# Kernel tuning notes

Measured on AMD Instinct MI355X. Metric: run time of the kernel, lower is better.

## Reference

```python
import jax, jax.numpy as jnp
import numpy as np

B, SQ, SK, D, H = 8, 1024, 1024, 1024, 16
DH = D // H  # attention head size = 64
LN_EPS = 1e-5


def _layer_norm(x, g, b):
    m = jnp.mean(x, axis=-1, keepdims=True)
    v = jnp.mean(jnp.square(x - m), axis=-1, keepdims=True)
    return (x - m) * jax.lax.rsqrt(v + LN_EPS) * g + b


def setup_inputs() -> dict:
    key = jax.random.key(0)
    ks = jax.random.split(key, 12)
    s = 0.02
    return {
        "hidden_states": jax.random.normal(ks[0], (B, SQ, D), jnp.float32),
        "context": jax.random.normal(ks[1], (B, SK, D), jnp.float32),
        "Wq": jax.random.normal(ks[2], (D, D), jnp.float32) * s,
        "bq": jnp.zeros((D,), jnp.float32),
        "Wk": jax.random.normal(ks[3], (D, D), jnp.float32) * s,
        "bk": jnp.zeros((D,), jnp.float32),
        "Wv": jax.random.normal(ks[4], (D, D), jnp.float32) * s,
        "bv": jnp.zeros((D,), jnp.float32),
        "Wobs": jax.random.normal(ks[5], (D, D), jnp.float32) * s,
        "bobs": jnp.zeros((D,), jnp.float32),
        "Wmat": jax.random.normal(ks[6], (D, D), jnp.float32) * s,
        "bmat": jnp.zeros((D,), jnp.float32),
        "ln_g": jnp.ones((D,), jnp.float32),
        "ln_b": jnp.zeros((D,), jnp.float32),
    }


def reference(hidden_states, context, Wq, bq, Wk, bk, Wv, bv,
              Wobs, bobs, Wmat, bmat, ln_g, ln_b):
    # QKV projections (torch Linear: x @ W.T + b)
    q = hidden_states @ Wq.T + bq            # [B, SQ, D]
    k = context @ Wk.T + bk                  # [B, SK, D]
    v = context @ Wv.T + bv                  # [B, SK, D]

    # ---- Guide_Block: single-head SDPA over full D, then linear->ReLU->LN ----
    # (dropout is identity in eval mode)
    score = jnp.einsum('bqd,bkd->bqk', q, k) / np.sqrt(D)   # [B, SQ, SK]
    attn = jax.nn.softmax(score, axis=-1)
    gctx = jnp.einsum('bqk,bkd->bqd', attn, v)              # [B, SQ, D]
    new_q = _layer_norm(jax.nn.relu(gctx @ Wobs.T + bobs), ln_g, ln_b)
    new_k = _layer_norm(jax.nn.relu(k @ Wmat.T + bmat), ln_g, ln_b)

    # ---- Multi-head attention with guided q/k and original v ----
    qh = new_q.reshape(B, SQ, H, DH).transpose(0, 2, 1, 3)  # [B, H, SQ, DH]
    kh = new_k.reshape(B, SK, H, DH).transpose(0, 2, 1, 3)
    vh = v.reshape(B, SK, H, DH).transpose(0, 2, 1, 3)
    scores = jnp.einsum('bhqd,bhkd->bhqk', qh, kh) / np.sqrt(DH)
    probs = jax.nn.softmax(scores, axis=-1)                 # attn dropout = identity (eval)
    out = jnp.einsum('bhqk,bhkd->bhqd', probs, vh)          # [B, H, SQ, DH]
    return out.transpose(0, 2, 1, 3).reshape(B, SQ, D)
```

## Files before the change

kernel.cpp:

```cpp
#include <hip/hip_runtime.h>
#include <hip/hip_bf16.h>

#define DEV __device__ __forceinline__

using bf16x8 = __attribute__((ext_vector_type(8))) short;
using f32x4  = __attribute__((ext_vector_type(4))) float;
using f32x16 = __attribute__((ext_vector_type(16))) float;

#define MFMA16(a, b, c) __builtin_amdgcn_mfma_f32_16x16x32_bf16((a), (b), (c), 0, 0, 0)
#define MFMA32(a, b, c) __builtin_amdgcn_mfma_f32_32x32x16_bf16((a), (b), (c), 0, 0, 0)

#define GLOAD_LDS16(gp, lp)                                                        \
  __builtin_amdgcn_global_load_lds(                                               \
      (__attribute__((address_space(1))) unsigned int*)(gp),                      \
      (__attribute__((address_space(3))) unsigned int*)(lp), 16, 0, 0)

DEV float b2f(unsigned short u) {
  union { float f; unsigned u; } x; x.u = ((unsigned)u) << 16; return x.f;
}
DEV unsigned short f2b(float f) {
  union { float f; unsigned u; } x; x.f = f;
  unsigned r = x.u + 0x7FFFu + ((x.u >> 16) & 1u);
  return (unsigned short)(r >> 16);
}
DEV unsigned short f2b_trunc(float f) {
  union { float f; unsigned u; } x; x.f = f;
  return (unsigned short)(x.u >> 16);
}

__global__ __launch_bounds__(256) void detect_kernel(
    const unsigned short* __restrict__ hs, int* __restrict__ flag) {
  __shared__ int red[4];
  const int t = threadIdx.x;
  const ushort4* p = (const ushort4*)hs;
  int cnt = 0;
#pragma unroll
  for (int j = 0; j < 16; j++) {
    ushort4 u = p[j * 256 + t];
    cnt += (((u.x >> 7) & 0xFF) == 0xFF) + (((u.y >> 7) & 0xFF) == 0xFF) +
           (((u.z >> 7) & 0xFF) == 0xFF) + (((u.w >> 7) & 0xFF) == 0xFF);
  }
#pragma unroll
  for (int off = 32; off >= 1; off >>= 1) cnt += __shfl_xor(cnt, off, 64);
  if ((t & 63) == 0) red[t >> 6] = cnt;
  __syncthreads();
  if (t == 0) flag[0] = (red[0] + red[1] + red[2] + red[3] >= 4) ? 1 : 0;
}

__global__ __launch_bounds__(256) void convert2_kernel(
    const void* __restrict__ s0, const void* __restrict__ s1,
    unsigned short* __restrict__ d0, unsigned short* __restrict__ d1,
    const int* __restrict__ flag) {
  const int bid = blockIdx.x;
  const void* src;
  unsigned short* dst;
  long off;
  if (bid < 8192) { src = s0; dst = d0; off = (long)bid * 1024; }
  else            { src = s1; dst = d1; off = (long)(bid - 8192) * 1024; }
  const long i = off + threadIdx.x * 4;
  ushort4 o;
  if (*flag) {
    float4 f = ((const float4*)src)[i >> 2];
    o.x = f2b(f.x); o.y = f2b(f.y); o.z = f2b(f.z); o.w = f2b(f.w);
  } else {
    o = ((const ushort4*)src)[i >> 2];
  }
  ((ushort4*)dst)[i >> 2] = o;
}

__global__ __launch_bounds__(256) void convert_w_kernel(
    const void* __restrict__ s0, const void* __restrict__ s1,
    const void* __restrict__ s2, const void* __restrict__ s3,
    const void* __restrict__ s4, unsigned short* __restrict__ dst,
    const int* __restrict__ flag) {
  const void* srcs[5] = {s0, s1, s2, s3, s4};
  const void* src = srcs[blockIdx.y];
  unsigned short* d = dst + (long)blockIdx.y * 1048576;
  const int i = (blockIdx.x * 256 + threadIdx.x) * 4;
  ushort4 o;
  if (*flag) {
    float4 f = ((const float4*)src)[i >> 2];
    o.x = f2b(f.x); o.y = f2b(f.y); o.z = f2b(f.z); o.w = f2b(f.w);
  } else {
    o = ((const ushort4*)src)[i >> 2];
  }
  ((ushort4*)d)[i >> 2] = o;
}

__global__ __launch_bounds__(256) void convert_vec_kernel(
    const void* __restrict__ s0, const void* __restrict__ s1,
    const void* __restrict__ s2, const void* __restrict__ s3,
    const void* __restrict__ s4, const void* __restrict__ s5,
    const void* __restrict__ s6, unsigned short* __restrict__ dst,
    const int* __restrict__ flag) {
  const void* srcs[7] = {s0, s1, s2, s3, s4, s5, s6};
  const void* src = srcs[blockIdx.x];
  unsigned short* d = dst + blockIdx.x * 1024;
  const int i = threadIdx.x * 4;
  ushort4 o;
  if (*flag) {
    float4 f = ((const float4*)src)[i >> 2];
    o.x = f2b(f.x); o.y = f2b(f.y); o.z = f2b(f.z); o.w = f2b(f.w);
  } else {
    o = ((const ushort4*)src)[i >> 2];
  }
  ((ushort4*)d)[i >> 2] = o;
}

template <int RELU, int OUTBF16, int BIAS, int SPLIT>
__global__ __launch_bounds__(256, 2) void gemm_bt_kernel(
    const unsigned short* __restrict__ A, const unsigned short* __restrict__ B,
    const unsigned short* __restrict__ bias, void* __restrict__ Cv,
    void* __restrict__ Cv2, int M, int N, int K, long sA_, long sB_, long sC_,
    float scale) {
  __shared__ unsigned short sA[2][128 * 32];
  __shared__ unsigned short sB[2][128 * 32];
  const int t = threadIdx.x;
  const int wave = t >> 6, lane = t & 63;
  const int quad = lane >> 4, col = lane & 15;
  const int wm = wave >> 1, wn = wave & 1;
  const long zb = blockIdx.z;
  const unsigned short* Ab = A + zb * sA_ + (long)blockIdx.x * 128 * K;
  const unsigned short* Bb = B + zb * sB_ + (long)blockIdx.y * 128 * K;
  const int r0 = t >> 2;
  const int c0 = (t & 3) * 8;

  f32x4 zz = {0.f, 0.f, 0.f, 0.f};
  f32x4 acc[4][4];
#pragma unroll
  for (int i = 0; i < 4; i++)
#pragma unroll
    for (int j = 0; j < 4; j++) acc[i][j] = zz;

  for (int k0 = 0; k0 < K; k0 += 64) {
    __syncthreads();
#pragma unroll
    for (int p = 0; p < 2; p++) {
      GLOAD_LDS16(Ab + (long)r0 * K + k0 + p * 32 + c0,        &sA[p][t * 8]);
      GLOAD_LDS16(Ab + (long)(64 + r0) * K + k0 + p * 32 + c0, &sA[p][2048 + t * 8]);
      GLOAD_LDS16(Bb + (long)r0 * K + k0 + p * 32 + c0,        &sB[p][t * 8]);
      GLOAD_LDS16(Bb + (long)(64 + r0) * K + k0 + p * 32 + c0, &sB[p][2048 + t * 8]);
    }
    __syncthreads();
#pragma unroll
    for (int p = 0; p < 2; p++) {
      bf16x8 af[4], bfr[4];
#pragma unroll
      for (int mi = 0; mi < 4; mi++)
        af[mi] = *(const bf16x8*)&sA[p][(wm * 64 + mi * 16 + col) * 32 + quad * 8];
#pragma unroll
      for (int ni = 0; ni < 4; ni++)
        bfr[ni] = *(const bf16x8*)&sB[p][(wn * 64 + ni * 16 + col) * 32 + quad * 8];
#pragma unroll
      for (int mi = 0; mi < 4; mi++)
#pragma unroll
        for (int ni = 0; ni < 4; ni++)
          acc[mi][ni] = MFMA16(af[mi], bfr[ni], acc[mi][ni]);
    }
  }

  const int Rm = blockIdx.x * 128 + wm * 64;
  const int Cn = blockIdx.y * 128 + wn * 64;
  float bs[4];
#pragma unroll
  for (int ni = 0; ni < 4; ni++)
    bs[ni] = BIAS ? b2f(bias[Cn + ni * 16 + col]) : 0.f;

  unsigned short* Cb = (unsigned short*)Cv;
  int Nw = N, cadj = 0;
  if (SPLIT) {
    Nw = N >> 1;
    if (blockIdx.y >= (gridDim.y >> 1)) { Cb = (unsigned short*)Cv2; cadj = Nw; }
  }
#pragma unroll
  for (int mi = 0; mi < 4; mi++)
#pragma unroll
    for (int ni = 0; ni < 4; ni++)
#pragma unroll
      for (int r = 0; r < 4; r++) {
        int rr = Rm + mi * 16 + quad * 4 + r;
        int cc = Cn + ni * 16 + col;
        float v = acc[mi][ni][r] * scale + bs[ni];
        if (RELU) v = fmaxf(v, 0.f);
        if (OUTBF16)
          Cb[zb * sC_ + (long)rr * Nw + (cc - cadj)] = f2b(v);
        else
          ((float*)Cv)[zb * sC_ + (long)rr * N + cc] = v;
      }
}

__global__ __launch_bounds__(256) void softmax_kernel(
    const float* __restrict__ S, unsigned short* __restrict__ P) {
  __shared__ float red[8];
  const long row = blockIdx.x;
  const int t = threadIdx.x;
  const float4 v4 = ((const float4*)(S + row * 1024))[t];
  float x[4] = {v4.x, v4.y, v4.z, v4.w};
  float m = fmaxf(fmaxf(x[0], x[1]), fmaxf(x[2], x[3]));
#pragma unroll
  for (int off = 32; off >= 1; off >>= 1) m = fmaxf(m, __shfl_xor(m, off, 64));
  if ((t & 63) == 0) red[t >> 6] = m;
  __syncthreads();
  m = fmaxf(fmaxf(red[0], red[1]), fmaxf(red[2], red[3]));
  float e[4], s = 0.f;
#pragma unroll
  for (int i = 0; i < 4; i++) { e[i] = __expf(x[i] - m); s += e[i]; }
#pragma unroll
  for (int off = 32; off >= 1; off >>= 1) s += __shfl_xor(s, off, 64);
  __syncthreads();
  if ((t & 63) == 0) red[4 + (t >> 6)] = s;
  __syncthreads();
  s = red[4] + red[5] + red[6] + red[7];
  float inv = 1.f / s;
  ushort4 o;
  o.x = f2b(e[0] * inv); o.y = f2b(e[1] * inv);
  o.z = f2b(e[2] * inv); o.w = f2b(e[3] * inv);
  ((ushort4*)(P + row * 1024))[t] = o;
}

DEV float block_sum(float v, float* red, int t) {
#pragma unroll
  for (int off = 32; off >= 1; off >>= 1) v += __shfl_xor(v, off, 64);
  __syncthreads();
  if ((t & 63) == 0) red[t >> 6] = v;
  __syncthreads();
  return red[0] + red[1] + red[2] + red[3];
}

__global__ __launch_bounds__(256) void layernorm2_kernel(
    const unsigned short* __restrict__ X0, const unsigned short* __restrict__ X1,
    const unsigned short* __restrict__ G, const unsigned short* __restrict__ Bt,
    unsigned short* __restrict__ Y0, unsigned short* __restrict__ Y1) {
  __shared__ float red[4];
  const int bid = blockIdx.x;
  const unsigned short* X;
  unsigned short* Y;
  if (bid < 8192) { X = X0 + (long)bid * 1024; Y = Y0 + (long)bid * 1024; }
  else { X = X1 + (long)(bid - 8192) * 1024; Y = Y1 + (long)(bid - 8192) * 1024; }
  const int t = threadIdx.x;
  ushort4 u = ((const ushort4*)X)[t];
  float x[4] = {b2f(u.x), b2f(u.y), b2f(u.z), b2f(u.w)};
  float s = x[0] + x[1] + x[2] + x[3];
  float mean = block_sum(s, red, t) * (1.f / 1024.f);
  float d0 = x[0] - mean, d1 = x[1] - mean, d2 = x[2] - mean, d3 = x[3] - mean;
  float vs = d0 * d0 + d1 * d1 + d2 * d2 + d3 * d3;
  float var = block_sum(vs, red, t) * (1.f / 1024.f);
  float rs = rsqrtf(var + 1e-5f);
  ushort4 gu = ((const ushort4*)G)[t];
  ushort4 bu = ((const ushort4*)Bt)[t];
  ushort4 o;
  o.x = f2b(d0 * rs * b2f(gu.x) + b2f(bu.x));
  o.y = f2b(d1 * rs * b2f(gu.y) + b2f(bu.y));
  o.z = f2b(d2 * rs * b2f(gu.z) + b2f(bu.z));
  o.w = f2b(d3 * rs * b2f(gu.w) + b2f(bu.w));
  ((ushort4*)Y)[t] = o;
}

__global__ __launch_bounds__(256) void transpose_kernel(
    const unsigned short* __restrict__ V, unsigned short* __restrict__ VT) {
  __shared__ unsigned short tile[32][33];
  const int b = blockIdx.z;
  const int d0 = blockIdx.x * 32, sk0 = blockIdx.y * 32;
  const int tx = threadIdx.x & 31, ty = threadIdx.x >> 5;
#pragma unroll
  for (int i = 0; i < 32; i += 8)
    tile[ty + i][tx] = V[((long)(b * 1024 + sk0 + ty + i)) * 1024 + d0 + tx];
  __syncthreads();
#pragma unroll
  for (int i = 0; i < 32; i += 8)
    VT[((long)(b * 1024 + d0 + ty + i)) * 1024 + sk0 + tx] = tile[tx][ty + i];
}

__global__ __launch_bounds__(256, 2) void flash_mha_kernel(
    const unsigned short* __restrict__ Q, const unsigned short* __restrict__ K,
    const unsigned short* __restrict__ VT, void* __restrict__ O,
    const int* __restrict__ flag) {
  __shared__ unsigned short sK[2][64 * 64];
  __shared__ unsigned short sV[2][64 * 64];
  __shared__ float lred[4][2][32];
  const int t = threadIdx.x;
  const int wave = t >> 6, lane = t & 63;
  const int lr = lane & 31, lh = lane >> 5;

  const int flat = blockIdx.x + (blockIdx.y << 2) + (blockIdx.z << 6);
  const int w = (flat & 7) * 64 + (flat >> 3);
  const int xq = w & 3, h = (w >> 2) & 15, b = w >> 6;
  const int q0 = xq * 256 + wave * 64;

  bf16x8 bq[2][4];
#pragma unroll
  for (int qt = 0; qt < 2; qt++)
#pragma unroll
    for (int d0 = 0; d0 < 4; d0++)
      bq[qt][d0] = *(const bf16x8*)(Q +
          ((long)(b * 1024 + q0 + qt * 32 + lr)) * 1024 + h * 64 + d0 * 16 + lh * 8);

  const unsigned short* Ks[2];
  const unsigned short* Vs[2];
#pragma unroll
  for (int j = 0; j < 2; j++) {
    const int i = t + j * 256;
    const int row = i >> 3;
    const int c = ((i & 7) ^ (row & 7)) * 8;
    const int prow = (row & ~12) | ((row & 4) << 1) | ((row & 8) >> 1);
    Ks[j] = K + ((long)(b * 1024 + prow)) * 1024 + h * 64 + c;
    Vs[j] = VT + ((long)(b * 1024 + h * 64 + row)) * 1024 + c;
  }
  const int lds0 = t * 8, lds1 = t * 8 + 2048;

#define STAGE(bi, kv0)                                        \
  {                                                           \
    GLOAD_LDS16(Ks[0] + (long)(kv0) * 1024, &sK[bi][lds0]);   \
    GLOAD_LDS16(Ks[1] + (long)(kv0) * 1024, &sK[bi][lds1]);   \
    GLOAD_LDS16(Vs[0] + (kv0), &sV[bi][lds0]);                \
    GLOAD_LDS16(Vs[1] + (kv0), &sV[bi][lds1]);                \
  }

  const f32x16 z16 = {0.f, 0.f, 0.f, 0.f, 0.f, 0.f, 0.f, 0.f,
                      0.f, 0.f, 0.f, 0.f, 0.f, 0.f, 0.f, 0.f};
  f32x16 o[2][2];
#pragma unroll
  for (int i = 0; i < 2; i++)
#pragma unroll
    for (int j = 0; j < 2; j++) o[i][j] = z16;
  float lsum[2] = {0.f, 0.f};

  STAGE(0, 0);
  for (int kt = 0; kt < 16; kt++) {
    const int bi = kt & 1;
    __syncthreads();
    if (kt < 15) STAGE(bi ^ 1, (kt + 1) * 64);

    f32x16 st[2][2];
#pragma unroll
    for (int i = 0; i < 2; i++)
#pragma unroll
      for (int j = 0; j < 2; j++) st[i][j] = z16;
#pragma unroll
    for (int kvt = 0; kvt < 2; kvt++) {
      const int krow = kvt * 32 + lr;
      const int kx = krow & 7;
#pragma unroll
      for (int d0 = 0; d0 < 4; d0++) {
        const bf16x8 kf =
            *(const bf16x8*)&sK[bi][krow * 64 + ((((d0 << 1) | lh) ^ kx) << 3)];
        st[0][kvt] = MFMA32(kf, bq[0][d0], st[0][kvt]);
        st[1][kvt] = MFMA32(kf, bq[1][d0], st[1][kvt]);
      }
    }

    bf16x8 pa[2][4];
#pragma unroll
    for (int qt = 0; qt < 2; qt++)
#pragma unroll
      for (int kvt = 0; kvt < 2; kvt++) {
        float e[16];
#pragma unroll
        for (int r = 0; r < 16; r++) {
          e[r] = exp2f(st[qt][kvt][r] * 0.18033688f);
          lsum[qt] += e[r];
        }
        unsigned dw[8];
#pragma unroll
        for (int m = 0; m < 8; m++)
          asm("v_cvt_pk_bf16_f32 %0, %1, %2"
              : "=v"(dw[m]) : "v"(e[2 * m]), "v"(e[2 * m + 1]));
        union { unsigned u[4]; bf16x8 v; } f0, f1;
        f0.u[0] = dw[0]; f0.u[1] = dw[1]; f0.u[2] = dw[2]; f0.u[3] = dw[3];
        f1.u[0] = dw[4]; f1.u[1] = dw[5]; f1.u[2] = dw[6]; f1.u[3] = dw[7];
        pa[qt][kvt * 2] = f0.v;
        pa[qt][kvt * 2 + 1] = f1.v;
      }

#pragma unroll
    for (int kc = 0; kc < 4; kc++)
#pragma unroll
      for (int dht = 0; dht < 2; dht++) {
        const int vrow = dht * 32 + lr;
        const bf16x8 vf =
            *(const bf16x8*)&sV[bi][vrow * 64 + ((((kc << 1) | lh) ^ (vrow & 7)) << 3)];
        o[0][dht] = MFMA32(pa[0][kc], vf, o[0][dht]);
        o[1][dht] = MFMA32(pa[1][kc], vf, o[1][dht]);
      }
  }
#undef STAGE

  float lt[2];
#pragma unroll
  for (int qt = 0; qt < 2; qt++)
    lt[qt] = lsum[qt] + __shfl_xor(lsum[qt], 32, 64);
  if (lane < 32) { lred[wave][0][lr] = lt[0]; lred[wave][1][lr] = lt[1]; }
  __syncthreads();

  const int f32o = *flag;
#pragma unroll
  for (int qt = 0; qt < 2; qt++)
#pragma unroll
    for (int r = 0; r < 16; r++) {
      const int rowi = (lh << 2) + (r & 3) + ((r >> 2) << 3);
      const float inv = 1.f / lred[wave][qt][rowi];
      const long gr =
          ((long)(b * 1024 + q0 + qt * 32 + rowi)) * 1024 + h * 64 + lr;
      if (f32o) {
        ((float*)O)[gr] = o[qt][0][r] * inv;
        ((float*)O)[gr + 32] = o[qt][1][r] * inv;
      } else {
        ((unsigned short*)O)[gr] = f2b(o[qt][0][r] * inv);
        ((unsigned short*)O)[gr + 32] = f2b(o[qt][1][r] * inv);
      }
    }
}

extern "C" void kernel_launch(void* const* d_in, const int* in_sizes, int n_in,
                              void* d_out, int out_size, void* d_ws,
                              size_t ws_size, hipStream_t stream) {
  (void)in_sizes; (void)n_in; (void)out_size; (void)ws_size;
  const void* hs   = d_in[0];
  const void* ctx  = d_in[1];
  const void* Wq   = d_in[2];
  const void* bq   = d_in[3];
  const void* Wk   = d_in[4];
  const void* bk   = d_in[5];
  const void* Wv   = d_in[6];
  const void* bv   = d_in[7];
  const void* Wobs = d_in[8];
  const void* bobs = d_in[9];
  const void* Wmat = d_in[10];
  const void* bmat = d_in[11];
  const void* lng  = d_in[12];
  const void* lnb  = d_in[13];

  const long E = 8LL * 1024 * 1024;
  const long W1 = 1024L * 1024L;
  unsigned short* base = (unsigned short*)d_ws;
  unsigned short* hsb   = base;
  unsigned short* ctxb  = base + E;
  unsigned short* Wb    = base + 2 * E;
  unsigned short* Wqb   = Wb;
  unsigned short* Wkb   = Wb + W1;
  unsigned short* Wvb   = Wb + 2 * W1;
  unsigned short* Wobsb = Wb + 3 * W1;
  unsigned short* Wmatb = Wb + 4 * W1;
  unsigned short* vecs  = base + 2 * E + 5 * W1;
  unsigned short* bqb   = vecs;
  unsigned short* bkb   = vecs + 1024;
  unsigned short* bvb   = vecs + 2048;
  unsigned short* bobsb = vecs + 3072;
  unsigned short* bmatb = vecs + 4096;
  unsigned short* lngb  = vecs + 5120;
  unsigned short* lnbb  = vecs + 6144;
  int* flag = (int*)(vecs + 32768);
  unsigned short* q     = vecs + W1;
  unsigned short* k     = q + E;
  unsigned short* v     = k + E;
  unsigned short* vT    = v + E;
  float* scores = (float*)(vT + E);
  unsigned short* nq    = (unsigned short*)scores;
  unsigned short* newq  = ((unsigned short*)scores) + E;
  unsigned short* probs = hsb;
  unsigned short* gctx  = ctxb;
  unsigned short* nk    = v;
  unsigned short* newk  = q;

  dim3 blk(256);
  const long S1 = 1024L * 1024L;

  detect_kernel<<<dim3(1), blk, 0, stream>>>((const unsigned short*)hs, flag);
  convert2_kernel<<<dim3(16384), blk, 0, stream>>>(hs, ctx, hsb, ctxb, flag);
  convert_w_kernel<<<dim3(1024, 5), blk, 0, stream>>>(Wq, Wk, Wv, Wobs, Wmat, Wb, flag);
  convert_vec_kernel<<<dim3(7), blk, 0, stream>>>(bq, bk, bv, bobs, bmat, lng, lnb,
                                                  vecs, flag);

  gemm_bt_kernel<0, 1, 1, 0><<<dim3(64, 8, 1), blk, 0, stream>>>(
      hsb, Wqb, bqb, q, q, 8192, 1024, 1024, 0, 0, 0, 1.f);
  gemm_bt_kernel<0, 1, 1, 1><<<dim3(64, 16, 1), blk, 0, stream>>>(
      ctxb, Wkb, bkb, k, v, 8192, 2048, 1024, 0, 0, 0, 1.f);
  transpose_kernel<<<dim3(32, 32, 8), blk, 0, stream>>>(v, vT);
  gemm_bt_kernel<0, 0, 0, 0><<<dim3(8, 8, 8), blk, 0, stream>>>(
      q, k, nullptr, scores, scores, 1024, 1024, 1024, S1, S1, S1, 0.03125f);
  softmax_kernel<<<dim3(8192), blk, 0, stream>>>(scores, probs);
  gemm_bt_kernel<0, 1, 0, 0><<<dim3(8, 8, 8), blk, 0, stream>>>(
      probs, vT, nullptr, gctx, gctx, 1024, 1024, 1024, S1, S1, S1, 1.f);
  gemm_bt_kernel<1, 1, 1, 0><<<dim3(64, 8, 1), blk, 0, stream>>>(
      gctx, Wobsb, bobsb, nq, nq, 8192, 1024, 1024, 0, 0, 0, 1.f);
  gemm_bt_kernel<1, 1, 1, 0><<<dim3(64, 8, 1), blk, 0, stream>>>(
      k, Wmatb, bmatb, nk, nk, 8192, 1024, 1024, 0, 0, 0, 1.f);
  layernorm2_kernel<<<dim3(16384), blk, 0, stream>>>(nq, nk, lngb, lnbb, newq, newk);
  flash_mha_kernel<<<dim3(4, 16, 8), blk, 0, stream>>>(
      newq, newk, vT, d_out, flag);
}
```

Before: 424.5 us.

## Halve per-wave query tile in flash MHA for higher occupancy, add setprio

Each wave in the final multi-head attention kernel now handles 32 query rows instead of 64. The grid doubles to 1024 blocks and launch bounds allow 4 blocks per CU, which cuts register pressure and raises occupancy. MFMA sections are wrapped in s_setprio to favour matrix issue, and the row sums are split into four accumulators. In exchange, K/V tiles are reloaded from global memory twice as often per query row and each LDS fragment feeds only one MFMA, which lowers reuse.

```diff
diff --git a/kernel.cpp b/kernel.cpp
--- a/kernel.cpp
+++ b/kernel.cpp
@@ -271,29 +271,27 @@
     VT[((long)(b * 1024 + d0 + ty + i)) * 1024 + sk0 + tx] = tile[tx][ty + i];
 }
 
-__global__ __launch_bounds__(256, 2) void flash_mha_kernel(
+__global__ __launch_bounds__(256, 4) void flash_mha_kernel(
     const unsigned short* __restrict__ Q, const unsigned short* __restrict__ K,
     const unsigned short* __restrict__ VT, void* __restrict__ O,
     const int* __restrict__ flag) {
   __shared__ unsigned short sK[2][64 * 64];
   __shared__ unsigned short sV[2][64 * 64];
-  __shared__ float lred[4][2][32];
+  __shared__ float lred[4][32];
   const int t = threadIdx.x;
   const int wave = t >> 6, lane = t & 63;
   const int lr = lane & 31, lh = lane >> 5;
 
-  const int flat = blockIdx.x + (blockIdx.y << 2) + (blockIdx.z << 6);
-  const int w = (flat & 7) * 64 + (flat >> 3);
-  const int xq = w & 3, h = (w >> 2) & 15, b = w >> 6;
-  const int q0 = xq * 256 + wave * 64;
-
-  bf16x8 bq[2][4];
-#pragma unroll
-  for (int qt = 0; qt < 2; qt++)
-#pragma unroll
-    for (int d0 = 0; d0 < 4; d0++)
-      bq[qt][d0] = *(const bf16x8*)(Q +
-          ((long)(b * 1024 + q0 + qt * 32 + lr)) * 1024 + h * 64 + d0 * 16 + lh * 8);
+  const int flat = blockIdx.x + (blockIdx.y << 3) + (blockIdx.z << 7);
+  const int w = (flat & 7) * 128 + (flat >> 3);
+  const int xq = w & 7, h = (w >> 3) & 15, b = w >> 7;
+  const int q0 = xq * 128 + wave * 32;
+
+  bf16x8 bq[4];
+#pragma unroll
+  for (int d0 = 0; d0 < 4; d0++)
+    bq[d0] = *(const bf16x8*)(Q +
+        ((long)(b * 1024 + q0 + lr)) * 1024 + h * 64 + d0 * 16 + lh * 8);
 
   const unsigned short* Ks[2];
   const unsigned short* Vs[2];
@@ -318,12 +316,9 @@
 
   const f32x16 z16 = {0.f, 0.f, 0.f, 0.f, 0.f, 0.f, 0.f, 0.f,
                       0.f, 0.f, 0.f, 0.f, 0.f, 0.f, 0.f, 0.f};
-  f32x16 o[2][2];
-#pragma unroll
-  for (int i = 0; i < 2; i++)
-#pragma unroll
-    for (int j = 0; j < 2; j++) o[i][j] = z16;
-  float lsum[2] = {0.f, 0.f};
+  f32x16 o[2];
+  o[0] = z16; o[1] = z16;
+  float p0 = 0.f, p1 = 0.f, p2 = 0.f, p3 = 0.f;
 
   STAGE(0, 0);
   for (int kt = 0; kt < 16; kt++) {
@@ -331,11 +326,9 @@
     __syncthreads();
     if (kt < 15) STAGE(bi ^ 1, (kt + 1) * 64);
 
-    f32x16 st[2][2];
-#pragma unroll
-    for (int i = 0; i < 2; i++)
-#pragma unroll
-      for (int j = 0; j < 2; j++) st[i][j] = z16;
+    f32x16 st[2];
+    st[0] = z16; st[1] = z16;
+    __builtin_amdgcn_s_setprio(1);
 #pragma unroll
     for (int kvt = 0; kvt < 2; kvt++) {
       const int krow = kvt * 32 + lr;
@@ -344,34 +337,35 @@
       for (int d0 = 0; d0 < 4; d0++) {
         const bf16x8 kf =
             *(const bf16x8*)&sK[bi][krow * 64 + ((((d0 << 1) | lh) ^ kx) << 3)];
-        st[0][kvt] = MFMA32(kf, bq[0][d0], st[0][kvt]);
-        st[1][kvt] = MFMA32(kf, bq[1][d0], st[1][kvt]);
+        st[kvt] = MFMA32(kf, bq[d0], st[kvt]);
       }
     }
-
-    bf16x8 pa[2][4];
-#pragma unroll
-    for (int qt = 0; qt < 2; qt++)
-#pragma unroll
-      for (int kvt = 0; kvt < 2; kvt++) {
-        float e[16];
-#pragma unroll
-        for (int r = 0; r < 16; r++) {
-          e[r] = exp2f(st[qt][kvt][r] * 0.18033688f);
-          lsum[qt] += e[r];
-        }
-        unsigned dw[8];
-#pragma unroll
-        for (int m = 0; m < 8; m++)
-          asm("v_cvt_pk_bf16_f32 %0, %1, %2"
-              : "=v"(dw[m]) : "v"(e[2 * m]), "v"(e[2 * m + 1]));
-        union { unsigned u[4]; bf16x8 v; } f0, f1;
-        f0.u[0] = dw[0]; f0.u[1] = dw[1]; f0.u[2] = dw[2]; f0.u[3] = dw[3];
-        f1.u[0] = dw[4]; f1.u[1] = dw[5]; f1.u[2] = dw[6]; f1.u[3] = dw[7];
-        pa[qt][kvt * 2] = f0.v;
-        pa[qt][kvt * 2 + 1] = f1.v;
+    __builtin_amdgcn_s_setprio(0);
+
+    bf16x8 pa[4];
+#pragma unroll
+    for (int kvt = 0; kvt < 2; kvt++) {
+      float e[16];
+#pragma unroll
+      for (int r = 0; r < 16; r++)
+        e[r] = exp2f(st[kvt][r] * 0.18033688f);
+#pragma unroll
+      for (int r = 0; r < 16; r += 4) {
+        p0 += e[r]; p1 += e[r + 1]; p2 += e[r + 2]; p3 += e[r + 3];
       }
-
+      unsigned dw[8];
+#pragma unroll
+      for (int m = 0; m < 8; m++)
+        asm("v_cvt_pk_bf16_f32 %0, %1, %2"
+            : "=v"(dw[m]) : "v"(e[2 * m]), "v"(e[2 * m + 1]));
+      union { unsigned u[4]; bf16x8 v; } f0, f1;
+      f0.u[0] = dw[0]; f0.u[1] = dw[1]; f0.u[2] = dw[2]; f0.u[3] = dw[3];
+      f1.u[0] = dw[4]; f1.u[1] = dw[5]; f1.u[2] = dw[6]; f1.u[3] = dw[7];
+      pa[kvt * 2] = f0.v;
+      pa[kvt * 2 + 1] = f1.v;
+    }
+
+    __builtin_amdgcn_s_setprio(1);
 #pragma unroll
     for (int kc = 0; kc < 4; kc++)
 #pragma unroll
@@ -379,36 +373,31 @@
         const int vrow = dht * 32 + lr;
         const bf16x8 vf =
             *(const bf16x8*)&sV[bi][vrow * 64 + ((((kc << 1) | lh) ^ (vrow & 7)) << 3)];
-        o[0][dht] = MFMA32(pa[0][kc], vf, o[0][dht]);
-        o[1][dht] = MFMA32(pa[1][kc], vf, o[1][dht]);
+        o[dht] = MFMA32(pa[kc], vf, o[dht]);
       }
+    __builtin_amdgcn_s_setprio(0);
   }
 #undef STAGE
 
-  float lt[2];
-#pragma unroll
-  for (int qt = 0; qt < 2; qt++)
-    lt[qt] = lsum[qt] + __shfl_xor(lsum[qt], 32, 64);
-  if (lane < 32) { lred[wave][0][lr] = lt[0]; lred[wave][1][lr] = lt[1]; }
+  float lt = (p0 + p1) + (p2 + p3);
+  lt += __shfl_xor(lt, 32, 64);
+  if (lane < 32) lred[wave][lr] = lt;
   __syncthreads();
 
   const int f32o = *flag;
 #pragma unroll
-  for (int qt = 0; qt < 2; qt++)
-#pragma unroll
-    for (int r = 0; r < 16; r++) {
-      const int rowi = (lh << 2) + (r & 3) + ((r >> 2) << 3);
-      const float inv = 1.f / lred[wave][qt][rowi];
-      const long gr =
-          ((long)(b * 1024 + q0 + qt * 32 + rowi)) * 1024 + h * 64 + lr;
-      if (f32o) {
-        ((float*)O)[gr] = o[qt][0][r] * inv;
-        ((float*)O)[gr + 32] = o[qt][1][r] * inv;
-      } else {
-        ((unsigned short*)O)[gr] = f2b(o[qt][0][r] * inv);
-        ((unsigned short*)O)[gr + 32] = f2b(o[qt][1][r] * inv);
-      }
+  for (int r = 0; r < 16; r++) {
+    const int rowi = (lh << 2) + (r & 3) + ((r >> 2) << 3);
+    const float inv = 1.f / lred[wave][rowi];
+    const long gr = ((long)(b * 1024 + q0 + rowi)) * 1024 + h * 64 + lr;
+    if (f32o) {
+      ((float*)O)[gr] = o[0][r] * inv;
+      ((float*)O)[gr + 32] = o[1][r] * inv;
+    } else {
+      ((unsigned short*)O)[gr] = f2b(o[0][r] * inv);
+      ((unsigned short*)O)[gr + 32] = f2b(o[1][r] * inv);
     }
+  }
 }
 
 extern "C" void kernel_launch(void* const* d_in, const int* in_sizes, int n_in,
@@ -486,6 +475,6 @@
   gemm_bt_kernel<1, 1, 1, 0><<<dim3(64, 8, 1), blk, 0, stream>>>(
       k, Wmatb, bmatb, nk, nk, 8192, 1024, 1024, 0, 0, 0, 1.f);
   layernorm2_kernel<<<dim3(16384), blk, 0, stream>>>(nq, nk, lngb, lnbb, newq, newk);
-  flash_mha_kernel<<<dim3(4, 16, 8), blk, 0, stream>>>(
+  flash_mha_kernel<<<dim3(8, 16, 8), blk, 0, stream>>>(
       newq, newk, vT, d_out, flag);
 }
```

After: 414.0 us. 2.5% less time.
